# Kernel tuning notes

Hardware: AMD Instinct MI355X
Metric: run time of the kernel (lower is better)

## Reference

```python
import jax, jax.numpy as jnp
import numpy as np

DIM = 256
NUM_HEADS = 8


def setup_inputs() -> dict:
    key = jax.random.key(0)
    ks = jax.random.split(key, 5)
    x = jax.random.normal(ks[0], (32, DIM, 56, 56), dtype=jnp.float32)
    # Conv2d(dim, 2*dim, k=1, groups=2): weight [2*dim, dim//2, 1, 1]
    qk_w = jax.random.normal(ks[1], (2 * DIM, DIM // 2, 1, 1), dtype=jnp.float32) * (DIM // 2) ** -0.5
    qk_b = jax.random.normal(ks[2], (2 * DIM,), dtype=jnp.float32) * 0.02
    # Conv2d(dim, dim, k=3, pad=1, groups=dim): weight [dim, 1, 3, 3]
    pe_w = jax.random.normal(ks[3], (DIM, 1, 3, 3), dtype=jnp.float32) * (1.0 / 3.0)
    pe_b = jax.random.normal(ks[4], (DIM,), dtype=jnp.float32) * 0.02
    return {"x": x, "qk_w": qk_w, "qk_b": qk_b, "pe_w": pe_w, "pe_b": pe_b}


def _conv(x, w, padding, groups):
    return jax.lax.conv_general_dilated(
        x, w, window_strides=(1, 1), padding=padding,
        feature_group_count=groups,
        dimension_numbers=("NCHW", "OIHW", "NCHW"))


def reference(x, qk_w, qk_b, pe_w, pe_b):
    b, c, h, w = x.shape
    H, hd = NUM_HEADS, c // NUM_HEADS
    n = h * w
    s = n ** (-0.5)

    # grouped 1x1 conv -> elu + 1 feature map
    qk = _conv(x, qk_w, "VALID", groups=2) + qk_b[None, :, None, None]
    qk = jax.nn.elu(qk) + 1.0                       # [b, 2c, h, w]
    qk = qk.reshape(b, 2, H, hd, n)
    q, k = qk[:, 0], qk[:, 1]                       # [b, H, hd, n]
    v = x.reshape(b, H, hd, n)                      # [b, H, hd, n]

    # kv = (k*s) @ (v^T * s)  -> [b, H, hd, hd]
    kv = jnp.einsum("bhdn,bhen->bhde", k * s, v * s)
    # numerator: q^T @ kv -> [b, H, n, hd]
    num = jnp.einsum("bhdn,bhde->bhne", q, kv)
    # denominator: q^T @ mean_n(k) -> [b, H, n]
    den = jnp.einsum("bhdn,bhd->bhn", q, k.mean(axis=-1))
    out = num / (den[..., None] + 1e-6)             # [b, H, n, hd]

    out = out.transpose(0, 1, 3, 2).reshape(b, c, h, w)
    pe = _conv(x, pe_w, [(1, 1), (1, 1)], groups=c) + pe_b[None, :, None, None]
    return out + pe
```

## Files before the change

### kernel.cpp

```cpp
#include <hip/hip_runtime.h>
#include <cmath>

#define NCH   256
#define NPIX  3136
#define NB    32
#define SEV   7
#define INV_N (1.0f / 3136.0f)

typedef __attribute__((ext_vector_type(8)))  short bf16x8;
typedef __attribute__((ext_vector_type(4)))  float f32x4;
typedef __attribute__((ext_vector_type(16))) float f32x16;

#define KV7_F  (SEV * NB * 8 * 1024)
#define KM7_F  (SEV * NB * 256)
#define KVF_F  (NB * 8 * 1024)
#define KMF_F  (NB * 256)
#define KM7_OFF (KV7_F)
#define KVF_OFF (KM7_OFF + KM7_F)
#define KMF_OFF (KVF_OFF + KVF_F)
#define WF_OFF  (KMF_OFF + KMF_F)

__device__ __forceinline__ ushort f2bf(float f) {
  unsigned u = __float_as_uint(f);
  u += 0x7FFFu + ((u >> 16) & 1u);
  return (ushort)(u >> 16);
}
__device__ __forceinline__ float bf2f(ushort h) {
  return __uint_as_float(((unsigned)h) << 16);
}

__global__ void wfrag_kernel(const float* __restrict__ qk_w, ushort* __restrict__ Wf) {
  const int tid = blockIdx.x * 512 + threadIdx.x;
  const int lane = tid & 63;
  const int ks = (tid >> 6) & 3;
  const int mt = (tid >> 8) & 15;
  const int hl = (tid >> 12) & 1;
  const int side = (tid >> 13) & 1;
  const int ch = mt * 16 + (lane & 15);
  const int oc = side * 256 + ch;
  ushort v[8];
#pragma unroll
  for (int j = 0; j < 8; ++j) {
    const int k = ks * 32 + (lane >> 4) * 8 + j;
    const float w = qk_w[(size_t)oc * 128 + k];
    const ushort hi = f2bf(w);
    v[j] = (hl == 0) ? hi : f2bf(w - bf2f(hi));
  }
  *(uint4*)(Wf + (size_t)tid * 8) = *(const uint4*)v;
}

__global__ __launch_bounds__(512, 4)
void kv_kernel(const float* __restrict__ x, const ushort* __restrict__ Wf,
               const float* __restrict__ qk_b, float* __restrict__ kv7,
               float* __restrict__ km7) {
  const int bid = blockIdx.x;
  const int hd = (bid >= 224) ? 1 : 0;
  const int rem = bid - hd * 224;
  const int sev = rem >> 5, b = rem & 31;
  const int t = threadIdx.x;
  const int w = t >> 6, l = t & 63;
  const int q = l >> 4, r15 = l & 15;
  const int e = l & 31, q5 = l >> 5;
  const int h_l = w & 3, ph = w >> 2;
  const int mt = w;

  __shared__ __align__(16) ushort Xb[64][152];
  __shared__ __align__(16) ushort KVs[2 * 128 * 88];
  ushort (*Kst)[88] = (ushort(*)[88])KVs;
  ushort (*Vst)[88] = (ushort(*)[88])(KVs + 128 * 88);

  bf16x8 wf[4][2];
#pragma unroll
  for (int ks = 0; ks < 4; ++ks)
#pragma unroll
    for (int hl = 0; hl < 2; ++hl) {
      const size_t off =
          (size_t)(((((2 + hl) * 16 + (hd * 8 + mt)) * 4 + ks) * 64 + l)) * 8;
      wf[ks][hl] = *(const bf16x8*)(Wf + off);
    }

  float bias[4];
#pragma unroll
  for (int r = 0; r < 4; ++r)
    bias[r] = qk_b[256 + hd * 128 + mt * 16 + q * 4 + r];

  f32x16 kvacc;
#pragma unroll
  for (int i = 0; i < 16; ++i) kvacc[i] = 0.f;
  float kmacc[4] = {0.f, 0.f, 0.f, 0.f};

  const float* xk = x + ((size_t)(b * NCH) + 128) * NPIX + sev * 448;
  const float* xv = x + ((size_t)(b * NCH)) * NPIX + sev * 448;

  for (int st = 0; st < SEV; ++st) {
    const int p0 = st * 64;
    __syncthreads();

#pragma unroll
    for (int rr = 0; rr < 4; ++rr) {
      const int id = t + 512 * rr;
      const int cc = id >> 4;
      const int pf = id & 15;
      const float4 v = *(const float4*)(xk + (size_t)cc * NPIX + p0 + pf * 4);
      const ushort b0 = f2bf(v.x), b1 = f2bf(v.y), b2 = f2bf(v.z), b3 = f2bf(v.w);
      Xb[pf * 4 + 0][cc] = b0;
      Xb[pf * 4 + 1][cc] = b1;
      Xb[pf * 4 + 2][cc] = b2;
      Xb[pf * 4 + 3][cc] = b3;
      if (hd == 1) {
        const uint2 pk = {(uint)b0 | ((uint)b1 << 16), (uint)b2 | ((uint)b3 << 16)};
        *(uint2*)&Vst[cc][pf * 4] = pk;
      }
    }
    if (hd == 0) {
#pragma unroll
      for (int rr = 0; rr < 4; ++rr) {
        const int id = t + 512 * rr;
        const int cc = id >> 4;
        const int pf = id & 15;
        const float4 v = *(const float4*)(xv + (size_t)cc * NPIX + p0 + pf * 4);
        const uint2 pk = {(uint)f2bf(v.x) | ((uint)f2bf(v.y) << 16),
                          (uint)f2bf(v.z) | ((uint)f2bf(v.w) << 16)};
        *(uint2*)&Vst[cc][pf * 4] = pk;
      }
    }
    __syncthreads();

    f32x4 acc[4];
#pragma unroll
    for (int nt = 0; nt < 4; ++nt)
#pragma unroll
      for (int r = 0; r < 4; ++r) acc[nt][r] = 0.f;
#pragma unroll
    for (int ks = 0; ks < 4; ++ks) {
      bf16x8 xbf[4];
#pragma unroll
      for (int nt = 0; nt < 4; ++nt)
        xbf[nt] = *(const bf16x8*)&Xb[nt * 16 + r15][ks * 32 + q * 8];
#pragma unroll
      for (int nt = 0; nt < 4; ++nt) {
        acc[nt] = __builtin_amdgcn_mfma_f32_16x16x32_bf16(wf[ks][0], xbf[nt], acc[nt], 0, 0, 0);
        acc[nt] = __builtin_amdgcn_mfma_f32_16x16x32_bf16(wf[ks][1], xbf[nt], acc[nt], 0, 0, 0);
      }
    }

#pragma unroll
    for (int nt = 0; nt < 4; ++nt) {
#pragma unroll
      for (int r = 0; r < 4; ++r) {
        float v = acc[nt][r] + bias[r];
        v = (v > 0.f) ? (v + 1.f) : __expf(v);
        kmacc[r] += v;
        Kst[mt * 16 + q * 4 + r][nt * 16 + r15] = f2bf(v);
      }
    }
    __syncthreads();

#pragma unroll
    for (int ks2 = 0; ks2 < 2; ++ks2) {
      const int kp = ph * 32 + ks2 * 16 + q5 * 8;
      const bf16x8 ak = *(const bf16x8*)&Kst[h_l * 32 + e][kp];
      const bf16x8 bv = *(const bf16x8*)&Vst[h_l * 32 + e][kp];
      kvacc = __builtin_amdgcn_mfma_f32_32x32x16_bf16(ak, bv, kvacc, 0, 0, 0);
    }
  }

  __syncthreads();
  float* red = (float*)KVs;
#pragma unroll
  for (int reg = 0; reg < 16; ++reg) {
    const int row = (reg & 3) + 8 * (reg >> 2) + 4 * q5;
    red[w * 1024 + row * 32 + e] = kvacc[reg];
  }
  __syncthreads();
#pragma unroll
  for (int i = 0; i < 8; ++i) {
    const int idx = t + 512 * i;
    const int hl2 = idx >> 10;
    const int el = idx & 1023;
    const float s = red[hl2 * 1024 + el] + red[(hl2 + 4) * 1024 + el];
    kv7[(((size_t)sev * NB + b) * 8 + hd * 4 + hl2) * 1024 + el] = s;
  }
#pragma unroll
  for (int r = 0; r < 4; ++r) {
    float s = kmacc[r];
    s += __shfl_xor(s, 1);
    s += __shfl_xor(s, 2);
    s += __shfl_xor(s, 4);
    s += __shfl_xor(s, 8);
    if (r15 == 0)
      km7[((size_t)sev * NB + b) * 256 + hd * 128 + mt * 16 + q * 4 + r] = s;
  }
}

__global__ void red_kernel(const float* __restrict__ kv7, const float* __restrict__ km7,
                           float* __restrict__ kvF, float* __restrict__ kmF) {
  const int b = blockIdx.x;
  const int t = threadIdx.x;
  for (int i = t; i < 8192; i += 256) {
    float s = 0.f;
#pragma unroll
    for (int sv = 0; sv < SEV; ++sv)
      s += kv7[(size_t)(sv * NB + b) * 8192 + i];
    kvF[(size_t)b * 8192 + i] = s * INV_N;
  }
  {
    float s = 0.f;
#pragma unroll
    for (int sv = 0; sv < SEV; ++sv)
      s += km7[(size_t)(sv * NB + b) * 256 + t];
    kmF[b * 256 + t] = s * INV_N;
  }
}

__global__ __launch_bounds__(512, 2)
void out_kernel(const float* __restrict__ x, const ushort* __restrict__ Wf,
                const float* __restrict__ qk_b, const float* __restrict__ kvF,
                const float* __restrict__ kmF, float* __restrict__ out) {
  const int bid = blockIdx.x;
  const int b = bid & 31, sev = bid >> 5;
  const int t = threadIdx.x;
  const int wave = t >> 6, l = t & 63;
  const int q = l >> 4, r15 = l & 15;
  const int mw = wave & 3, ng = wave >> 2;
  const int h = wave;

  __shared__ ushort Xb[64][136];
  __shared__ ushort QT[64][264];
  __shared__ float denT[8][64];

  bf16x8 wf[4][4][2];
#pragma unroll
  for (int mti = 0; mti < 4; ++mti)
#pragma unroll
    for (int ks = 0; ks < 4; ++ks)
#pragma unroll
      for (int hl = 0; hl < 2; ++hl) {
        const size_t off =
            (size_t)((((hl * 16 + (mw * 4 + mti)) * 4 + ks) * 64 + l)) * 8;
        wf[mti][ks][hl] = *(const bf16x8*)(Wf + off);
      }

  float bias[4][4], kmw[4][4];
#pragma unroll
  for (int mti = 0; mti < 4; ++mti)
#pragma unroll
    for (int r = 0; r < 4; ++r) {
      const int c = (mw * 4 + mti) * 16 + q * 4 + r;
      bias[mti][r] = qk_b[c];
      kmw[mti][r] = kmF[b * 256 + c];
    }

  bf16x8 bkv[2];
#pragma unroll
  for (int eh = 0; eh < 2; ++eh) {
#pragma unroll
    for (int j = 0; j < 8; ++j)
      bkv[eh][j] = (short)f2bf(
          kvF[(size_t)b * 8192 + h * 1024 + (q * 8 + j) * 32 + eh * 16 + r15]);
  }

  const float* xq = x + (size_t)(b * NCH) * NPIX + sev * 448;

  for (int st = 0; st < SEV; ++st) {
    const int pos0 = st * 64;
#pragma unroll
    for (int rr = 0; rr < 4; ++rr) {
      const int id = t + 512 * rr;
      const int ch = id >> 4;
      const int p4 = (id & 15) * 4;
      const float4 v = *(const float4*)(xq + (size_t)ch * NPIX + pos0 + p4);
      Xb[p4 + 0][ch] = f2bf(v.x);
      Xb[p4 + 1][ch] = f2bf(v.y);
      Xb[p4 + 2][ch] = f2bf(v.z);
      Xb[p4 + 3][ch] = f2bf(v.w);
    }
    __syncthreads();

    f32x4 acc[4][2];
#pragma unroll
    for (int i = 0; i < 4; ++i)
#pragma unroll
      for (int nt = 0; nt < 2; ++nt)
#pragma unroll
        for (int r = 0; r < 4; ++r) acc[i][nt][r] = 0.f;
#pragma unroll
    for (int ks = 0; ks < 4; ++ks) {
      const bf16x8 xb0 = *(const bf16x8*)&Xb[(ng * 2 + 0) * 16 + r15][ks * 32 + q * 8];
      const bf16x8 xb1 = *(const bf16x8*)&Xb[(ng * 2 + 1) * 16 + r15][ks * 32 + q * 8];
#pragma unroll
      for (int mti = 0; mti < 4; ++mti) {
        acc[mti][0] = __builtin_amdgcn_mfma_f32_16x16x32_bf16(wf[mti][ks][0], xb0, acc[mti][0], 0, 0, 0);
        acc[mti][0] = __builtin_amdgcn_mfma_f32_16x16x32_bf16(wf[mti][ks][1], xb0, acc[mti][0], 0, 0, 0);
        acc[mti][1] = __builtin_amdgcn_mfma_f32_16x16x32_bf16(wf[mti][ks][0], xb1, acc[mti][1], 0, 0, 0);
        acc[mti][1] = __builtin_amdgcn_mfma_f32_16x16x32_bf16(wf[mti][ks][1], xb1, acc[mti][1], 0, 0, 0);
      }
    }

    float pdh[2][2];
    pdh[0][0] = pdh[0][1] = pdh[1][0] = pdh[1][1] = 0.f;
#pragma unroll
    for (int mti = 0; mti < 4; ++mti) {
#pragma unroll
      for (int nt = 0; nt < 2; ++nt) {
        ushort pk[4];
        float dsum = 0.f;
#pragma unroll
        for (int r = 0; r < 4; ++r) {
          float v = acc[mti][nt][r] + bias[mti][r];
          v = (v > 0.f) ? (v + 1.f) : __expf(v);
          pk[r] = f2bf(v);
          dsum += v * kmw[mti][r];
        }
        *(uint2*)&QT[(ng * 2 + nt) * 16 + r15][(mw * 4 + mti) * 16 + q * 4] =
            *(const uint2*)pk;
        pdh[mti >> 1][nt] += dsum;
      }
    }
#pragma unroll
    for (int ht = 0; ht < 2; ++ht)
#pragma unroll
      for (int nt = 0; nt < 2; ++nt) {
        float s = pdh[ht][nt];
        s += __shfl_xor(s, 16);
        s += __shfl_xor(s, 32);
        if (q == 0) denT[mw * 2 + ht][(ng * 2 + nt) * 16 + r15] = s;
      }
    __syncthreads();

#pragma unroll
    for (int pt = 0; pt < 4; ++pt) {
      const bf16x8 aq = *(const bf16x8*)&QT[pt * 16 + r15][h * 32 + q * 8];
      f32x4 z;
      z[0] = z[1] = z[2] = z[3] = 0.f;
      const f32x4 n0 = __builtin_amdgcn_mfma_f32_16x16x32_bf16(aq, bkv[0], z, 0, 0, 0);
      const f32x4 n1 = __builtin_amdgcn_mfma_f32_16x16x32_bf16(aq, bkv[1], z, 0, 0, 0);
      float4 o0, o1;
      float rdn[4];
#pragma unroll
      for (int r = 0; r < 4; ++r)
        rdn[r] = 1.0f / (denT[h][pt * 16 + q * 4 + r] + 1e-6f);
      o0.x = n0[0] * rdn[0]; o0.y = n0[1] * rdn[1];
      o0.z = n0[2] * rdn[2]; o0.w = n0[3] * rdn[3];
      o1.x = n1[0] * rdn[0]; o1.y = n1[1] * rdn[1];
      o1.z = n1[2] * rdn[2]; o1.w = n1[3] * rdn[3];
      const int posg = sev * 448 + pos0 + pt * 16 + q * 4;
      const int c0 = h * 32 + r15;
      const int c1 = h * 32 + 16 + r15;
      *(float4*)(out + ((size_t)(b * NCH + c0)) * NPIX + posg) = o0;
      *(float4*)(out + ((size_t)(b * NCH + c1)) * NPIX + posg) = o1;
    }
  }
}

__global__ __launch_bounds__(512, 4)
void pe_kernel(const float* __restrict__ x, const float* __restrict__ pe_w,
               const float* __restrict__ pe_b, float* __restrict__ out) {
  const int b = blockIdx.y;
  const int c0 = blockIdx.x * 4;
  const int t = threadIdx.x;
  const int wave = t >> 6;
  const int cl = wave & 3;
  const int rh = wave >> 2;
  const int lane = t & 63;

  __shared__ float xs[4][NPIX];

#pragma unroll
  for (int cc = 0; cc < 4; ++cc) {
    const float4* src = (const float4*)(x + ((size_t)(b * NCH + c0 + cc)) * NPIX);
    float4* dst = (float4*)&xs[cc][0];
    for (int i = t; i < NPIX / 4; i += 512) dst[i] = src[i];
  }
  __syncthreads();

  const int c = c0 + cl;
  float pw[9];
#pragma unroll
  for (int i = 0; i < 9; ++i) pw[i] = pe_w[c * 9 + i];
  const float pb = pe_b[c];
  float* oc = out + ((size_t)(b * NCH + c)) * NPIX;
  const float* xc = xs[cl];

  if (lane < 56) {
    const bool hasL = (lane > 0), hasR = (lane < 55);
    for (int rg = 0; rg < 7; ++rg) {
      const int rbase = rh * 28 + rg * 4;
      float o[4];
#pragma unroll
      for (int k = 0; k < 4; ++k) o[k] = oc[(rbase + k) * 56 + lane];
#pragma unroll
      for (int k = 0; k < 4; ++k) {
        const int r = rbase + k;
        float s = pb;
#pragma unroll
        for (int dy = -1; dy <= 1; ++dy) {
          const int rr = r + dy;
          if (rr < 0 || rr >= 56) continue;
          const float* xrow = xc + rr * 56 + lane;
          if (hasL) s += pw[(dy + 1) * 3 + 0] * xrow[-1];
          s += pw[(dy + 1) * 3 + 1] * xrow[0];
          if (hasR) s += pw[(dy + 1) * 3 + 2] * xrow[1];
        }
        o[k] += s;
      }
#pragma unroll
      for (int k = 0; k < 4; ++k) oc[(rbase + k) * 56 + lane] = o[k];
    }
  }
}

extern "C" void kernel_launch(void* const* d_in, const int* in_sizes, int n_in,
                              void* d_out, int out_size, void* d_ws,
                              size_t ws_size, hipStream_t stream) {
  const float* x    = (const float*)d_in[0];
  const float* qk_w = (const float*)d_in[1];
  const float* qk_b = (const float*)d_in[2];
  const float* pe_w = (const float*)d_in[3];
  const float* pe_b = (const float*)d_in[4];
  float* out = (float*)d_out;

  float* wsf = (float*)d_ws;
  float* kv7 = wsf;
  float* km7 = wsf + KM7_OFF;
  float* kvF = wsf + KVF_OFF;
  float* kmF = wsf + KMF_OFF;
  ushort* Wf = (ushort*)(wsf + WF_OFF);

  wfrag_kernel<<<32, 512, 0, stream>>>(qk_w, Wf);
  kv_kernel<<<448, 512, 0, stream>>>(x, Wf, qk_b, kv7, km7);
  red_kernel<<<NB, 256, 0, stream>>>(kv7, km7, kvF, kmF);
  out_kernel<<<SEV * NB, 512, 0, stream>>>(x, Wf, qk_b, kvF, kmF, out);

  dim3 g3(64, NB);
  pe_kernel<<<g3, 512, 0, stream>>>(x, pe_w, pe_b, out);
}
```

Measured before the change: 166.2 us.

## Split out_kernel across head halves to double grid and cut register use

The output kernel is split so each block computes only half of the heads (128 of 256 q channels), doubling the grid from 224 to 448 blocks. Per-thread register arrays for weight fragments, bias and kv shrink by about 4x, and launch bounds rise to 4 blocks per CU for higher occupancy. The cost is that every x tile is loaded and converted to bf16 twice, once per head-half, which adds global reads and conversion work. The denominator partials are now summed from two rows of shared memory.

After: 151.2 us. -9.1%, faster.

```diff
diff --git a/kernel.cpp b/kernel.cpp
--- a/kernel.cpp
+++ b/kernel.cpp
@@ -213,51 +213,49 @@
   }
 }
 
-__global__ __launch_bounds__(512, 2)
+__global__ __launch_bounds__(512, 4)
 void out_kernel(const float* __restrict__ x, const ushort* __restrict__ Wf,
                 const float* __restrict__ qk_b, const float* __restrict__ kvF,
                 const float* __restrict__ kmF, float* __restrict__ out) {
   const int bid = blockIdx.x;
-  const int b = bid & 31, sev = bid >> 5;
+  const int hd = (bid >= 224) ? 1 : 0;
+  const int rem = bid - hd * 224;
+  const int b = rem & 31, sev = rem >> 5;
   const int t = threadIdx.x;
-  const int wave = t >> 6, l = t & 63;
+  const int w = t >> 6, l = t & 63;
   const int q = l >> 4, r15 = l & 15;
-  const int mw = wave & 3, ng = wave >> 2;
-  const int h = wave;
+  const int mt = w;
+  const int h_l = w & 3, eh = w >> 2;
 
   __shared__ ushort Xb[64][136];
-  __shared__ ushort QT[64][264];
-  __shared__ float denT[8][64];
-
-  bf16x8 wf[4][4][2];
-#pragma unroll
-  for (int mti = 0; mti < 4; ++mti)
-#pragma unroll
-    for (int ks = 0; ks < 4; ++ks)
-#pragma unroll
-      for (int hl = 0; hl < 2; ++hl) {
-        const size_t off =
-            (size_t)((((hl * 16 + (mw * 4 + mti)) * 4 + ks) * 64 + l)) * 8;
-        wf[mti][ks][hl] = *(const bf16x8*)(Wf + off);
-      }
-
-  float bias[4][4], kmw[4][4];
-#pragma unroll
-  for (int mti = 0; mti < 4; ++mti)
-#pragma unroll
-    for (int r = 0; r < 4; ++r) {
-      const int c = (mw * 4 + mti) * 16 + q * 4 + r;
-      bias[mti][r] = qk_b[c];
-      kmw[mti][r] = kmF[b * 256 + c];
-    }
-
-  bf16x8 bkv[2];
-#pragma unroll
-  for (int eh = 0; eh < 2; ++eh) {
+  __shared__ ushort QT[64][136];
+  __shared__ float denP[8][64];
+
+  bf16x8 wf[4][2];
+#pragma unroll
+  for (int ks = 0; ks < 4; ++ks)
+#pragma unroll
+    for (int hl = 0; hl < 2; ++hl) {
+      const size_t off =
+          (size_t)((((hl * 16 + (hd * 8 + mt)) * 4 + ks) * 64 + l)) * 8;
+      wf[ks][hl] = *(const bf16x8*)(Wf + off);
+    }
+
+  float bias[4], kmw[4];
+#pragma unroll
+  for (int r = 0; r < 4; ++r) {
+    const int c = hd * 128 + mt * 16 + q * 4 + r;
+    bias[r] = qk_b[c];
+    kmw[r] = kmF[b * 256 + c];
+  }
+
+  bf16x8 bkv;
+  {
+    const int hg = hd * 4 + h_l;
 #pragma unroll
     for (int j = 0; j < 8; ++j)
-      bkv[eh][j] = (short)f2bf(
-          kvF[(size_t)b * 8192 + h * 1024 + (q * 8 + j) * 32 + eh * 16 + r15]);
+      bkv[j] = (short)f2bf(
+          kvF[(size_t)b * 8192 + hg * 1024 + (q * 8 + j) * 32 + eh * 16 + r15]);
   }
 
   const float* xq = x + (size_t)(b * NCH) * NPIX + sev * 448;
@@ -277,78 +275,60 @@
     }
     __syncthreads();
 
-    f32x4 acc[4][2];
-#pragma unroll
-    for (int i = 0; i < 4; ++i)
-#pragma unroll
-      for (int nt = 0; nt < 2; ++nt)
-#pragma unroll
-        for (int r = 0; r < 4; ++r) acc[i][nt][r] = 0.f;
+    f32x4 acc[4];
+#pragma unroll
+    for (int nt = 0; nt < 4; ++nt)
+#pragma unroll
+      for (int r = 0; r < 4; ++r) acc[nt][r] = 0.f;
 #pragma unroll
     for (int ks = 0; ks < 4; ++ks) {
-      const bf16x8 xb0 = *(const bf16x8*)&Xb[(ng * 2 + 0) * 16 + r15][ks * 32 + q * 8];
-      const bf16x8 xb1 = *(const bf16x8*)&Xb[(ng * 2 + 1) * 16 + r15][ks * 32 + q * 8];
-#pragma unroll
-      for (int mti = 0; mti < 4; ++mti) {
-        acc[mti][0] = __builtin_amdgcn_mfma_f32_16x16x32_bf16(wf[mti][ks][0], xb0, acc[mti][0], 0, 0, 0);
-        acc[mti][0] = __builtin_amdgcn_mfma_f32_16x16x32_bf16(wf[mti][ks][1], xb0, acc[mti][0], 0, 0, 0);
-        acc[mti][1] = __builtin_amdgcn_mfma_f32_16x16x32_bf16(wf[mti][ks][0], xb1, acc[mti][1], 0, 0, 0);
-        acc[mti][1] = __builtin_amdgcn_mfma_f32_16x16x32_bf16(wf[mti][ks][1], xb1, acc[mti][1], 0, 0, 0);
-      }
-    }
-
-    float pdh[2][2];
-    pdh[0][0] = pdh[0][1] = pdh[1][0] = pdh[1][1] = 0.f;
-#pragma unroll
-    for (int mti = 0; mti < 4; ++mti) {
-#pragma unroll
-      for (int nt = 0; nt < 2; ++nt) {
-        ushort pk[4];
-        float dsum = 0.f;
-#pragma unroll
-        for (int r = 0; r < 4; ++r) {
-          float v = acc[mti][nt][r] + bias[mti][r];
-          v = (v > 0.f) ? (v + 1.f) : __expf(v);
-          pk[r] = f2bf(v);
-          dsum += v * kmw[mti][r];
-        }
-        *(uint2*)&QT[(ng * 2 + nt) * 16 + r15][(mw * 4 + mti) * 16 + q * 4] =
-            *(const uint2*)pk;
-        pdh[mti >> 1][nt] += dsum;
-      }
-    }
-#pragma unroll
-    for (int ht = 0; ht < 2; ++ht)
-#pragma unroll
-      for (int nt = 0; nt < 2; ++nt) {
-        float s = pdh[ht][nt];
-        s += __shfl_xor(s, 16);
-        s += __shfl_xor(s, 32);
-        if (q == 0) denT[mw * 2 + ht][(ng * 2 + nt) * 16 + r15] = s;
-      }
+      bf16x8 xbf[4];
+#pragma unroll
+      for (int nt = 0; nt < 4; ++nt)
+        xbf[nt] = *(const bf16x8*)&Xb[nt * 16 + r15][ks * 32 + q * 8];
+#pragma unroll
+      for (int nt = 0; nt < 4; ++nt) {
+        acc[nt] = __builtin_amdgcn_mfma_f32_16x16x32_bf16(wf[ks][0], xbf[nt], acc[nt], 0, 0, 0);
+        acc[nt] = __builtin_amdgcn_mfma_f32_16x16x32_bf16(wf[ks][1], xbf[nt], acc[nt], 0, 0, 0);
+      }
+    }
+
+#pragma unroll
+    for (int nt = 0; nt < 4; ++nt) {
+      ushort pk[4];
+      float dsum = 0.f;
+#pragma unroll
+      for (int r = 0; r < 4; ++r) {
+        float v = acc[nt][r] + bias[r];
+        v = (v > 0.f) ? (v + 1.f) : __expf(v);
+        pk[r] = f2bf(v);
+        dsum += v * kmw[r];
+      }
+      *(uint2*)&QT[nt * 16 + r15][mt * 16 + q * 4] = *(const uint2*)pk;
+      dsum += __shfl_xor(dsum, 16);
+      dsum += __shfl_xor(dsum, 32);
+      if (q == 0) denP[mt][nt * 16 + r15] = dsum;
+    }
     __syncthreads();
 
 #pragma unroll
     for (int pt = 0; pt < 4; ++pt) {
-      const bf16x8 aq = *(const bf16x8*)&QT[pt * 16 + r15][h * 32 + q * 8];
+      const bf16x8 aq = *(const bf16x8*)&QT[pt * 16 + r15][h_l * 32 + q * 8];
       f32x4 z;
       z[0] = z[1] = z[2] = z[3] = 0.f;
-      const f32x4 n0 = __builtin_amdgcn_mfma_f32_16x16x32_bf16(aq, bkv[0], z, 0, 0, 0);
-      const f32x4 n1 = __builtin_amdgcn_mfma_f32_16x16x32_bf16(aq, bkv[1], z, 0, 0, 0);
-      float4 o0, o1;
+      const f32x4 n0 = __builtin_amdgcn_mfma_f32_16x16x32_bf16(aq, bkv, z, 0, 0, 0);
+      float4 o0;
       float rdn[4];
 #pragma unroll
-      for (int r = 0; r < 4; ++r)
-        rdn[r] = 1.0f / (denT[h][pt * 16 + q * 4 + r] + 1e-6f);
+      for (int r = 0; r < 4; ++r) {
+        const int pl = pt * 16 + q * 4 + r;
+        rdn[r] = 1.0f / (denP[2 * h_l][pl] + denP[2 * h_l + 1][pl] + 1e-6f);
+      }
       o0.x = n0[0] * rdn[0]; o0.y = n0[1] * rdn[1];
       o0.z = n0[2] * rdn[2]; o0.w = n0[3] * rdn[3];
-      o1.x = n1[0] * rdn[0]; o1.y = n1[1] * rdn[1];
-      o1.z = n1[2] * rdn[2]; o1.w = n1[3] * rdn[3];
       const int posg = sev * 448 + pos0 + pt * 16 + q * 4;
-      const int c0 = h * 32 + r15;
-      const int c1 = h * 32 + 16 + r15;
-      *(float4*)(out + ((size_t)(b * NCH + c0)) * NPIX + posg) = o0;
-      *(float4*)(out + ((size_t)(b * NCH + c1)) * NPIX + posg) = o1;
+      const int c = hd * 128 + h_l * 32 + eh * 16 + r15;
+      *(float4*)(out + ((size_t)(b * NCH + c)) * NPIX + posg) = o0;
     }
   }
 }
@@ -430,7 +410,7 @@
   wfrag_kernel<<<32, 512, 0, stream>>>(qk_w, Wf);
   kv_kernel<<<448, 512, 0, stream>>>(x, Wf, qk_b, kv7, km7);
   red_kernel<<<NB, 256, 0, stream>>>(kv7, km7, kvF, kmF);
-  out_kernel<<<SEV * NB, 512, 0, stream>>>(x, Wf, qk_b, kvF, kmF, out);
+  out_kernel<<<448, 512, 0, stream>>>(x, Wf, qk_b, kvF, kmF, out);
 
   dim3 g3(64, NB);
   pe_kernel<<<g3, 512, 0, stream>>>(x, pe_w, pe_b, out);
```
